# Optimization experiments

Hardware: AMD Instinct MI355X
Metric: run time of the kernel (lower is better)

## Reference

```python
import jax, jax.numpy as jnp
import numpy as np

N = 256  # image box size
B, P, L = 32, 300000, 64


def _gauss_kernel(sigma=1.0, size=5):
    ax = np.arange(size) - size // 2
    g = np.exp(-(ax ** 2) / (2.0 * sigma ** 2))
    k = np.outer(g, g)
    k = k / k.sum()
    return jnp.asarray(k, jnp.float32)


def _splat(cx, cy, w):
    # bilinear scatter-splat of P weighted points into [B, N, N] images
    x0 = jnp.floor(cx)
    y0 = jnp.floor(cy)
    fx = cx - x0
    fy = cy - y0
    xi0 = jnp.clip(x0.astype(jnp.int32), 0, N - 1)
    yi0 = jnp.clip(y0.astype(jnp.int32), 0, N - 1)
    xi1 = jnp.clip(xi0 + 1, 0, N - 1)
    yi1 = jnp.clip(yi0 + 1, 0, N - 1)
    b = jnp.broadcast_to(jnp.arange(cx.shape[0])[:, None], cx.shape)
    img = jnp.zeros((cx.shape[0], N, N), cx.dtype)
    img = img.at[b, yi0, xi0].add(w * (1 - fx) * (1 - fy))
    img = img.at[b, yi0, xi1].add(w * fx * (1 - fy))
    img = img.at[b, yi1, xi0].add(w * (1 - fx) * fy)
    img = img.at[b, yi1, xi1].add(w * fx * fy)
    return img


def setup_inputs() -> dict:
    key = jax.random.key(0)
    ks = jax.random.split(key, 9)
    z_x = jax.random.normal(ks[0], (B, L), jnp.float32)
    z_y = jax.random.normal(ks[1], (B, L), jnp.float32)
    z_z = jax.random.normal(ks[2], (B, L), jnp.float32)
    # Zernike basis scaled so deformations are a few pixels
    Z = 0.05 * jax.random.normal(ks[3], (P, L), jnp.float32)
    # masked volume point coordinates, centered, within +-N/4
    coords = (jax.random.uniform(ks[4], (P, 3), jnp.float32) - 0.5) * (0.5 * N)
    weights = jax.random.uniform(ks[5], (P,), jnp.float32)
    # proper per-image rotation matrices from random Euler angles (zyz)
    rng = np.random.RandomState(0)
    ang = rng.uniform(-np.pi, np.pi, (B, 3))
    ca, sa = np.cos(ang), np.sin(ang)
    Rm = np.zeros((B, 3, 3), np.float32)
    for i in range(B):
        a, b2, g = ang[i]
        Rz1 = np.array([[np.cos(a), -np.sin(a), 0], [np.sin(a), np.cos(a), 0], [0, 0, 1]])
        Ry = np.array([[np.cos(b2), 0, np.sin(b2)], [0, 1, 0], [-np.sin(b2), 0, np.cos(b2)]])
        Rz2 = np.array([[np.cos(g), -np.sin(g), 0], [np.sin(g), np.cos(g), 0], [0, 0, 1]])
        Rm[i] = (Rz1 @ Ry @ Rz2).astype(np.float32)
    R = jnp.asarray(Rm)
    shifts = 5.0 * jax.random.normal(ks[6], (B, 2), jnp.float32)
    # per-image radial CTF filter in Fourier space
    f = np.fft.fftfreq(N).astype(np.float32)
    r2 = f[:, None] ** 2 + f[None, :] ** 2  # [N, N]
    df = rng.uniform(500.0, 1500.0, (B, 1, 1)).astype(np.float32)
    ctf = jnp.asarray(np.sin(np.pi * df * r2[None]), jnp.float32)
    return {"z_x": z_x, "z_y": z_y, "z_z": z_z, "Z": Z, "coords": coords,
            "weights": weights, "R": R, "shifts": shifts, "ctf": ctf}


def reference(z_x, z_y, z_z, Z, coords, weights, R, shifts, ctf):
    # computeDeformationField: d = z @ Z^T -> [B, P]
    d_x = z_x @ Z.T
    d_y = z_y @ Z.T
    d_z = z_z @ Z.T
    # applyDeformationField: add reference coordinates per axis
    c_x = coords[:, 0][None, :] + d_x
    c_y = coords[:, 1][None, :] + d_y
    c_z = coords[:, 2][None, :] + d_z
    # applyAlignmentMatrix: per-image rotation, keep projected x/y rows
    c_r_x = R[:, 0, 0:1] * c_x + R[:, 0, 1:2] * c_y + R[:, 0, 2:3] * c_z
    c_r_y = R[:, 1, 0:1] * c_x + R[:, 1, 1:2] * c_y + R[:, 1, 2:3] * c_z
    # applyShifts: per-image shift + box-center offset
    half = jnp.float32(N / 2)
    px = c_r_x + shifts[:, 0:1] + half
    py = c_r_y + shifts[:, 1:2] + half
    # scatterImgByPass: bilinear scatter splat
    w = jnp.broadcast_to(weights[None, :], px.shape)
    img = _splat(px, py, w)  # [B, N, N]
    # gaussianFilterImage: 5x5 Gaussian blur
    k = _gauss_kernel()
    img_f = jax.lax.conv_general_dilated(
        img[:, None], k[None, None], (1, 1), 'SAME',
        dimension_numbers=('NCHW', 'OIHW', 'NCHW'))[:, 0]
    # ctfFilterImage: FFT multiply by real CTF, inverse FFT
    ft = jnp.fft.fft2(img_f)
    out = jnp.real(jnp.fft.ifft2(ft * ctf.astype(ft.dtype)))
    return out
```

## Files before the change

kernel.cpp:

```cpp
#include <hip/hip_runtime.h>
#include <hip/hip_bf16.h>

#define NIMG 32
#define NPTS 300000
#define NL   64
#define NBOX 256

#define BANDS  4
#define BROWS  64
#define CHUNKS 2
#define CHPTS  (NPTS / CHUNKS)

#define WQS  2047.0f
#define WQI  (1.0f / 2047.0f)

typedef float v2f __attribute__((ext_vector_type(2)));
typedef unsigned long long u64;

__device__ __forceinline__ int rev8(int x) { return (int)(__brev((unsigned)x) >> 24); }

__global__ __launch_bounds__(256) void zero_kernel(float4* p, int n4) {
    int i = blockIdx.x * 256 + threadIdx.x;
    if (i < n4) p[i] = make_float4(0.f, 0.f, 0.f, 0.f);
}

__global__ __launch_bounds__(256) void uvprep_kernel(
    const float* __restrict__ z_x, const float* __restrict__ z_y,
    const float* __restrict__ z_z, const float* __restrict__ R,
    const float* __restrict__ shifts,
    float* __restrict__ ubuf, float* __restrict__ vbuf, float4* __restrict__ hdrbuf)
{
    int t = threadIdx.x;
    for (int e = t; e < NIMG * NL; e += 256) {
        int b = e >> 6;
        const float* Rb = R + b * 9;
        float zx = z_x[e], zy = z_y[e], zz = z_z[e];
        ubuf[e] = Rb[0] * zx + Rb[1] * zy + Rb[2] * zz;
        vbuf[e] = Rb[3] * zx + Rb[4] * zy + Rb[5] * zz;
    }
    if (t < NIMG) {
        const float* Rb = R + t * 9;
        hdrbuf[2 * t]     = make_float4(Rb[0], Rb[1], Rb[2], shifts[2 * t]     + 128.f);
        hdrbuf[2 * t + 1] = make_float4(Rb[3], Rb[4], Rb[5], shifts[2 * t + 1] + 128.f);
    }
}

__global__ __launch_bounds__(256) void project_kernel(
    const float* __restrict__ Zb, const float* __restrict__ coords,
    const float* __restrict__ weights,
    const float* __restrict__ ubuf, const float* __restrict__ vbuf,
    const float4* __restrict__ hdrbuf,
    u64* __restrict__ recs)
{
    int tid = threadIdx.x;
    int p = blockIdx.x * 256 + tid;
    if (p >= NPTS) return;

    v2f zr[32];
    {
        const float4* Zr4 = (const float4*)(Zb + (size_t)p * NL);
        float4 tmp[16];
        #pragma unroll
        for (int i = 0; i < 16; ++i) tmp[i] = Zr4[i];
        const v2f* t2 = (const v2f*)tmp;
        #pragma unroll
        for (int i = 0; i < 32; ++i) zr[i] = t2[i];
    }

    float cx0 = coords[3 * p + 0];
    float cy0 = coords[3 * p + 1];
    float cz0 = coords[3 * p + 2];
    float w   = weights[p];

    for (int b = 0; b < NIMG; ++b) {
        float4 h0 = hdrbuf[2 * b], h1 = hdrbuf[2 * b + 1];
        const v2f* u2 = (const v2f*)(ubuf + b * NL);
        const v2f* v2 = (const v2f*)(vbuf + b * NL);
        v2f ax = {0.f, 0.f}, ay = {0.f, 0.f};
        #pragma unroll
        for (int i = 0; i < 32; ++i) {
            ax += u2[i] * zr[i];
            ay += v2[i] * zr[i];
        }
        float px = fmaf(h0.x, cx0, fmaf(h0.y, cy0, fmaf(h0.z, cz0, h0.w))) + ax.x + ax.y;
        float py = fmaf(h1.x, cx0, fmaf(h1.y, cy0, fmaf(h1.z, cz0, h1.w))) + ay.x + ay.y;

        float x0f = floorf(px), y0f = floorf(py);
        float fx = px - x0f, fy = py - y0f;
        int xi0 = min(max((int)x0f, 0), NBOX - 1);
        int yi0 = min(max((int)y0f, 0), NBOX - 1);
        float w00 = w * (1.f - fx) * (1.f - fy);
        float w10 = w * fx * (1.f - fy);
        float w01 = w * (1.f - fx) * fy;
        float w11 = w * fx * fy;
        if (xi0 == NBOX - 1) {
            w00 += w10; w10 = 0.f;
            w01 += w11; w11 = 0.f;
        }
        if (yi0 == NBOX - 1) {
            w00 += w01; w01 = 0.f;
            w10 += w11; w11 = 0.f;
        }
        u64 rec = (u64)(unsigned)(xi0 | (yi0 << 8))
                | ((u64)(unsigned)(w00 * WQS + 0.5f) << 16)
                | ((u64)(unsigned)(w10 * WQS + 0.5f) << 28)
                | ((u64)(unsigned)(w01 * WQS + 0.5f) << 40)
                | ((u64)(unsigned)(w11 * WQS + 0.5f) << 52);
        recs[(size_t)b * NPTS + p] = rec;
    }
}

__global__ __launch_bounds__(1024) void splat2_kernel(
    const u64* __restrict__ recs, float* __restrict__ img)
{
    __shared__ u64 VA[32 * 128];
    __shared__ u64 VB[32 * 129];
    __shared__ u64 VC[32 * 128];
    __shared__ u64 VD[32 * 129];
    int tid = threadIdx.x;
    int id = blockIdx.x;
    int band = id >> 6;
    int g    = id & 63;
    int b = g >> 1, c = g & 1;

    for (int i = tid; i < 32 * 128; i += 1024) { VA[i] = 0ULL; VC[i] = 0ULL; }
    for (int i = tid; i < 32 * 129; i += 1024) { VB[i] = 0ULL; VD[i] = 0ULL; }
    __syncthreads();

    const int y_lo = band * BROWS;
    const u64* rp = recs + (size_t)b * NPTS + (size_t)c * CHPTS;

    for (int i = 4 * tid; i < CHPTS; i += 4096) {
        ulonglong2 R01 = *(const ulonglong2*)(rp + i);
        ulonglong2 R23 = *(const ulonglong2*)(rp + i + 2);
        u64 Ra[4] = {R01.x, R01.y, R23.x, R23.y};
        #pragma unroll
        for (int k = 0; k < 4; ++k) {
            u64 rec = Ra[k];
            unsigned ps = (unsigned)rec & 0xFFFFu;
            int xi0 = ps & 255;
            int yi0 = ps >> 8;
            int r0 = yi0 - y_lo;
            if ((unsigned)r0 >= BROWS) continue;
            u64 val = ((rec >> 16) & 0xFFFULL)
                    | (((rec >> 28) & 0xFFFULL) << 16)
                    | (((rec >> 40) & 0xFFFULL) << 32)
                    | (((rec >> 52) & 0xFFFULL) << 48);
            int qr = r0 >> 1;
            int qc = (xi0 + (xi0 & 1)) >> 1;
            bool xodd = (xi0 & 1), yodd = (r0 & 1);
            u64* base = yodd ? (xodd ? VD : VC) : (xodd ? VB : VA);
            int stride = xodd ? 129 : 128;
            atomicAdd(&base[qr * stride + qc], val);
        }
    }
    __syncthreads();
    int nrows = min(BROWS + 1, NBOX - y_lo);
    float* ib = img + (size_t)b * NBOX * NBOX + (size_t)y_lo * NBOX;
    for (int i = tid; i < nrows * NBOX; i += 1024) {
        int r = i >> 8, x = i & 255;
        int fc0 = x & 1;
        int fc1 = fc0 ^ 1;
        int ja = x >> 1;
        int jb = (x + 1) >> 1;
        unsigned acc = 0;
        if (r < BROWS) {
            int fr = (r & 1) << 1;
            acc += (unsigned)((VA[(r >> 1) * 128 + ja] >> (16 * (fr | fc0))) & 0xFFFFu);
            acc += (unsigned)((VB[(r >> 1) * 129 + jb] >> (16 * (fr | fc1))) & 0xFFFFu);
        }
        if (r >= 1) {
            int fr = ((r & 1) ^ 1) << 1;
            acc += (unsigned)((VC[((r - 1) >> 1) * 128 + ja] >> (16 * (fr | fc0))) & 0xFFFFu);
            acc += (unsigned)((VD[((r - 1) >> 1) * 129 + jb] >> (16 * (fr | fc1))) & 0xFFFFu);
        }
        if (acc) unsafeAtomicAdd(ib + i, (float)acc * WQI);
    }
}

__global__ __launch_bounds__(256) void splat_kernel(
    const float* __restrict__ z_x, const float* __restrict__ z_y,
    const float* __restrict__ z_z, const float* __restrict__ Zb,
    const float* __restrict__ coords, const float* __restrict__ weights,
    const float* __restrict__ R, const float* __restrict__ shifts,
    float* __restrict__ img)
{
    __shared__ float s_z[3][NIMG][NL];
    __shared__ float s_R[NIMG][9];
    __shared__ float s_sh[NIMG][2];

    int tid = threadIdx.x;
    for (int i = tid; i < NIMG * NL; i += 256) {
        (&s_z[0][0][0])[i] = z_x[i];
        (&s_z[1][0][0])[i] = z_y[i];
        (&s_z[2][0][0])[i] = z_z[i];
    }
    for (int i = tid; i < NIMG * 9; i += 256) (&s_R[0][0])[i] = R[i];
    if (tid < NIMG * 2) (&s_sh[0][0])[tid] = shifts[tid];
    __syncthreads();

    int p = blockIdx.x * 256 + tid;
    if (p >= NPTS) return;

    float4 zr[16];
    const float4* Zr4 = (const float4*)(Zb + (size_t)p * NL);
    #pragma unroll
    for (int i = 0; i < 16; ++i) zr[i] = Zr4[i];

    float cx0 = coords[3 * p + 0];
    float cy0 = coords[3 * p + 1];
    float cz0 = coords[3 * p + 2];
    float w   = weights[p];

    for (int b = 0; b < NIMG; ++b) {
        const float4* zx4 = (const float4*)s_z[0][b];
        const float4* zy4 = (const float4*)s_z[1][b];
        const float4* zz4 = (const float4*)s_z[2][b];
        float dx = 0.f, dy = 0.f, dz = 0.f;
        #pragma unroll
        for (int i = 0; i < 16; ++i) {
            float4 a = zx4[i];
            dx += a.x * zr[i].x + a.y * zr[i].y + a.z * zr[i].z + a.w * zr[i].w;
            float4 bb = zy4[i];
            dy += bb.x * zr[i].x + bb.y * zr[i].y + bb.z * zr[i].z + bb.w * zr[i].w;
            float4 c = zz4[i];
            dz += c.x * zr[i].x + c.y * zr[i].y + c.z * zr[i].z + c.w * zr[i].w;
        }
        float cx = cx0 + dx, cy = cy0 + dy, cz = cz0 + dz;
        const float* Rb = s_R[b];
        float px = Rb[0] * cx + Rb[1] * cy + Rb[2] * cz + s_sh[b][0] + 128.0f;
        float py = Rb[3] * cx + Rb[4] * cy + Rb[5] * cz + s_sh[b][1] + 128.0f;

        float x0 = floorf(px), y0 = floorf(py);
        float fx = px - x0, fy = py - y0;
        int xi0 = min(max((int)x0, 0), NBOX - 1);
        int yi0 = min(max((int)y0, 0), NBOX - 1);
        int xi1 = min(xi0 + 1, NBOX - 1);
        int yi1 = min(yi0 + 1, NBOX - 1);

        float* ib = img + (size_t)b * NBOX * NBOX;
        unsafeAtomicAdd(ib + yi0 * NBOX + xi0, w * (1.f - fx) * (1.f - fy));
        unsafeAtomicAdd(ib + yi0 * NBOX + xi1, w * fx * (1.f - fy));
        unsafeAtomicAdd(ib + yi1 * NBOX + xi0, w * (1.f - fx) * fy);
        unsafeAtomicAdd(ib + yi1 * NBOX + xi1, w * fx * fy);
    }
}

__device__ __forceinline__ void fft_dif_t(float2* s, const float2* tw, int t) {
    #pragma unroll
    for (int st = 7; st >= 0; --st) {
        int half = 1 << st;
        int j  = t & (half - 1);
        int i1 = ((t >> st) << (st + 1)) + j;
        int i2 = i1 + half;
        float2 a = s[i1], b = s[i2];
        float2 w = tw[j << (7 - st)];
        float dxr = a.x - b.x, dxi = a.y - b.y;
        s[i1] = make_float2(a.x + b.x, a.y + b.y);
        s[i2] = make_float2(w.x * dxr - w.y * dxi, w.x * dxi + w.y * dxr);
        __syncthreads();
    }
}

__device__ __forceinline__ void fft_dit_t(float2* s, const float2* tw, int t) {
    #pragma unroll
    for (int st = 0; st < 8; ++st) {
        int half = 1 << st;
        int j  = t & (half - 1);
        int i1 = ((t >> st) << (st + 1)) + j;
        int i2 = i1 + half;
        float2 a = s[i1], b = s[i2];
        float2 w = tw[j << (7 - st)];
        float cs = w.x, sn = -w.y;
        float tr = cs * b.x - sn * b.y;
        float ti = cs * b.y + sn * b.x;
        s[i1] = make_float2(a.x + tr, a.y + ti);
        s[i2] = make_float2(a.x - tr, a.y - ti);
        __syncthreads();
    }
}

__device__ __forceinline__ void fft_dif_soa(float* re, float* im, const float2* tw, int t) {
    #pragma unroll
    for (int st = 7; st >= 0; --st) {
        int half = 1 << st;
        int j  = t & (half - 1);
        int i1 = ((t >> st) << (st + 1)) + j;
        int i2 = i1 + half;
        float ar = re[i1], ai = im[i1], br = re[i2], bi = im[i2];
        float2 w = tw[j << (7 - st)];
        float dr = ar - br, di = ai - bi;
        re[i1] = ar + br;  im[i1] = ai + bi;
        re[i2] = w.x * dr - w.y * di;
        im[i2] = w.x * di + w.y * dr;
        __syncthreads();
    }
}

__device__ __forceinline__ void fft_dit_soa(float* re, float* im, const float2* tw, int t) {
    #pragma unroll
    for (int st = 0; st < 8; ++st) {
        int half = 1 << st;
        int j  = t & (half - 1);
        int i1 = ((t >> st) << (st + 1)) + j;
        int i2 = i1 + half;
        float ar = re[i1], ai = im[i1], br = re[i2], bi = im[i2];
        float2 w = tw[j << (7 - st)];
        float cs = w.x, sn = -w.y;
        float tr = cs * br - sn * bi;
        float ti = cs * bi + sn * br;
        re[i1] = ar + tr;  im[i1] = ai + ti;
        re[i2] = ar - tr;  im[i2] = ai - ti;
        __syncthreads();
    }
}

__device__ __forceinline__ void init_tw(float2* tw, int tid) {
    if (tid < 128) {
        float sn, cs;
        sincosf(-6.283185307179586f * (float)tid * (1.0f / 256.0f), &sn, &cs);
        tw[tid] = make_float2(cs, sn);
    }
}

__global__ __launch_bounds__(256) void fft_rows_fwd_blur_kernel(const float* __restrict__ img,
                                                                float2* __restrict__ freq)
{
    __shared__ float2 s[2][NBOX];
    __shared__ float  sb[2][NBOX];
    __shared__ float2 tw[128];
    int tid = threadIdx.x;
    int tx = tid & 127, ty = tid >> 7;
    init_tw(tw, tid);
    int row = blockIdx.x * 2 + ty;
    int b = row >> 8, y = row & (NBOX - 1);
    const float* ib = img + ((size_t)b << 16);
    const float gw[5] = {0.0544886845f, 0.2442013420f, 0.4026199469f,
                         0.2442013420f, 0.0544886845f};
    float acc0 = 0.f, acc1 = 0.f;
    #pragma unroll
    for (int dy = -2; dy <= 2; ++dy) {
        int yy = y + dy;
        if ((unsigned)yy < (unsigned)NBOX) {
            const float* rp = ib + yy * NBOX;
            acc0 += gw[dy + 2] * rp[tx];
            acc1 += gw[dy + 2] * rp[tx + 128];
        }
    }
    sb[ty][tx] = acc0;  sb[ty][tx + 128] = acc1;
    __syncthreads();
    float r0 = 0.f, r1 = 0.f;
    #pragma unroll
    for (int dx = -2; dx <= 2; ++dx) {
        int x0 = tx + dx, x1 = tx + 128 + dx;
        if ((unsigned)x0 < (unsigned)NBOX) r0 += gw[dx + 2] * sb[ty][x0];
        if ((unsigned)x1 < (unsigned)NBOX) r1 += gw[dx + 2] * sb[ty][x1];
    }
    s[ty][tx]       = make_float2(r0, 0.f);
    s[ty][tx + 128] = make_float2(r1, 0.f);
    __syncthreads();
    fft_dif_t(s[ty], tw, tx);
    float2* op = freq + (size_t)row * NBOX;
    op[tx]       = s[ty][tx];
    op[tx + 128] = s[ty][tx + 128];
}

__global__ __launch_bounds__(1024) void fft_cols_ctf8_kernel(float2* __restrict__ freq,
                                                             const float* __restrict__ ctf)
{
    __shared__ float  s_re[8][257];
    __shared__ float  s_im[8][257];
    __shared__ float2 tw[128];
    int tid = threadIdx.x;
    init_tw(tw, tid);
    int col = tid & 7, j = tid >> 3;
    int blk = blockIdx.x;
    int b = blk >> 5;
    int x = ((blk & 31) << 3) + col;
    float2* base = freq + ((size_t)b << 16) + x;

    float2 v0 = base[(size_t)j * NBOX];
    float2 v1 = base[(size_t)(j + 128) * NBOX];
    s_re[col][j] = v0.x;        s_im[col][j] = v0.y;
    s_re[col][j + 128] = v1.x;  s_im[col][j + 128] = v1.y;
    __syncthreads();

    fft_dif_soa(s_re[col], s_im[col], tw, j);

    const float* cb = ctf + ((size_t)b << 16) + rev8(x);
    float c0 = cb[rev8(j) * NBOX];
    float c1 = cb[rev8(j + 128) * NBOX];
    s_re[col][j] *= c0;        s_im[col][j] *= c0;
    s_re[col][j + 128] *= c1;  s_im[col][j + 128] *= c1;
    __syncthreads();

    fft_dit_soa(s_re[col], s_im[col], tw, j);

    const float inv = 1.0f / 256.0f;
    base[(size_t)j * NBOX]         = make_float2(s_re[col][j] * inv, s_im[col][j] * inv);
    base[(size_t)(j + 128) * NBOX] = make_float2(s_re[col][j + 128] * inv, s_im[col][j + 128] * inv);
}

__global__ __launch_bounds__(256) void fft_rows_inv_kernel(const float2* __restrict__ freq,
                                                           float* __restrict__ out)
{
    __shared__ float2 s[2][NBOX];
    __shared__ float2 tw[128];
    int tid = threadIdx.x;
    int tx = tid & 127, ty = tid >> 7;
    init_tw(tw, tid);
    int row = blockIdx.x * 2 + ty;
    const float2* rp = freq + (size_t)row * NBOX;
    s[ty][tx]       = rp[tx];
    s[ty][tx + 128] = rp[tx + 128];
    __syncthreads();
    fft_dit_t(s[ty], tw, tx);
    const float inv = 1.0f / 256.0f;
    out[(size_t)row * NBOX + tx]       = s[ty][tx].x * inv;
    out[(size_t)row * NBOX + tx + 128] = s[ty][tx + 128].x * inv;
}

extern "C" void kernel_launch(void* const* d_in, const int* in_sizes, int n_in,
                              void* d_out, int out_size, void* d_ws, size_t ws_size,
                              hipStream_t stream)
{
    (void)in_sizes; (void)n_in; (void)out_size;
    const float* z_x     = (const float*)d_in[0];
    const float* z_y     = (const float*)d_in[1];
    const float* z_z     = (const float*)d_in[2];
    const float* Zb      = (const float*)d_in[3];
    const float* coords  = (const float*)d_in[4];
    const float* weights = (const float*)d_in[5];
    const float* R       = (const float*)d_in[6];
    const float* shifts  = (const float*)d_in[7];
    const float* ctf     = (const float*)d_in[8];
    float* out = (float*)d_out;

    const size_t NELEM = (size_t)NIMG * NBOX * NBOX;
    const size_t NPAIR = (size_t)NIMG * NPTS;
    char* base = (char*)d_ws;
    float* img  = (float*)base;
    u64*   recs = (u64*)(base + 8388608);
    float* ubuf = (float*)(base + 8388608 + 76800000);
    float* vbuf = ubuf + NIMG * NL;
    float4* hdrbuf = (float4*)(vbuf + NIMG * NL);
    float2* freq = (float2*)(base + 8388608);
    const size_t required = 8388608 + 76800000 + NIMG * NL * 8 + NIMG * 2 * 16;

    zero_kernel<<<(int)(NELEM / 4 + 255) / 256, 256, 0, stream>>>((float4*)img, (int)(NELEM / 4));

    if (ws_size >= required) {
        uvprep_kernel<<<1, 256, 0, stream>>>(z_x, z_y, z_z, R, shifts, ubuf, vbuf, hdrbuf);
        project_kernel<<<(NPTS + 255) / 256, 256, 0, stream>>>(Zb, coords, weights,
                                                               ubuf, vbuf, hdrbuf, recs);
        splat2_kernel<<<NIMG * BANDS * CHUNKS, 1024, 0, stream>>>(recs, img);
    } else {
        splat_kernel<<<(NPTS + 255) / 256, 256, 0, stream>>>(z_x, z_y, z_z, Zb, coords,
                                                             weights, R, shifts, img);
    }

    fft_rows_fwd_blur_kernel<<<NIMG * NBOX / 2, 256, 0, stream>>>(img, freq);
    fft_cols_ctf8_kernel<<<NIMG * 32, 1024, 0, stream>>>(freq, ctf);
    fft_rows_inv_kernel<<<NIMG * NBOX / 2, 256, 0, stream>>>(freq, out);
}
```

Measured before the change: 167.1 us.

## Compute point deformations with bf16 MFMA matrix cores instead of scalar FMAs

```diff
diff --git a/kernel.cpp b/kernel.cpp
--- a/kernel.cpp
+++ b/kernel.cpp
@@ -15,9 +15,17 @@
 #define WQI  (1.0f / 2047.0f)
 
 typedef float v2f __attribute__((ext_vector_type(2)));
+typedef float f32x4 __attribute__((ext_vector_type(4)));
+typedef short bf16x8 __attribute__((ext_vector_type(8)));
 typedef unsigned long long u64;
 
 __device__ __forceinline__ int rev8(int x) { return (int)(__brev((unsigned)x) >> 24); }
+
+__device__ __forceinline__ short f2bf(float f) {
+    unsigned u = __float_as_uint(f);
+    unsigned r = (u + 0x7FFFu + ((u >> 16) & 1u)) >> 16;
+    return (short)r;
+}
 
 __global__ __launch_bounds__(256) void zero_kernel(float4* p, int n4) {
     int i = blockIdx.x * 256 + threadIdx.x;
@@ -28,85 +36,130 @@
     const float* __restrict__ z_x, const float* __restrict__ z_y,
     const float* __restrict__ z_z, const float* __restrict__ R,
     const float* __restrict__ shifts,
-    float* __restrict__ ubuf, float* __restrict__ vbuf, float4* __restrict__ hdrbuf)
-{
+    float4* __restrict__ hdrbuf, short* __restrict__ Bt)
+{
+    __shared__ float s_u[NIMG * NL];
+    __shared__ float s_v[NIMG * NL];
     int t = threadIdx.x;
     for (int e = t; e < NIMG * NL; e += 256) {
         int b = e >> 6;
         const float* Rb = R + b * 9;
         float zx = z_x[e], zy = z_y[e], zz = z_z[e];
-        ubuf[e] = Rb[0] * zx + Rb[1] * zy + Rb[2] * zz;
-        vbuf[e] = Rb[3] * zx + Rb[4] * zy + Rb[5] * zz;
+        s_u[e] = Rb[0] * zx + Rb[1] * zy + Rb[2] * zz;
+        s_v[e] = Rb[3] * zx + Rb[4] * zy + Rb[5] * zz;
     }
     if (t < NIMG) {
         const float* Rb = R + t * 9;
         hdrbuf[2 * t]     = make_float4(Rb[0], Rb[1], Rb[2], shifts[2 * t]     + 128.f);
         hdrbuf[2 * t + 1] = make_float4(Rb[3], Rb[4], Rb[5], shifts[2 * t + 1] + 128.f);
     }
-}
-
-__global__ __launch_bounds__(256) void project_kernel(
+    __syncthreads();
+    for (int e = t; e < 64 * NL; e += 256) {
+        int c = e >> 6, k = e & 63;
+        int b = c >> 1;
+        float val = (c & 1) ? s_v[b * NL + k] : s_u[b * NL + k];
+        Bt[e] = f2bf(val);
+    }
+}
+
+__device__ __forceinline__ u64 make_rec(float px, float py, float w) {
+    float x0f = floorf(px), y0f = floorf(py);
+    float fx = px - x0f, fy = py - y0f;
+    int xi0 = min(max((int)x0f, 0), NBOX - 1);
+    int yi0 = min(max((int)y0f, 0), NBOX - 1);
+    float w00 = w * (1.f - fx) * (1.f - fy);
+    float w10 = w * fx * (1.f - fy);
+    float w01 = w * (1.f - fx) * fy;
+    float w11 = w * fx * fy;
+    if (xi0 == NBOX - 1) {
+        w00 += w10; w10 = 0.f;
+        w01 += w11; w11 = 0.f;
+    }
+    if (yi0 == NBOX - 1) {
+        w00 += w01; w01 = 0.f;
+        w10 += w11; w11 = 0.f;
+    }
+    return (u64)(unsigned)(xi0 | (yi0 << 8))
+         | ((u64)(unsigned)(w00 * WQS + 0.5f) << 16)
+         | ((u64)(unsigned)(w10 * WQS + 0.5f) << 28)
+         | ((u64)(unsigned)(w01 * WQS + 0.5f) << 40)
+         | ((u64)(unsigned)(w11 * WQS + 0.5f) << 52);
+}
+
+__global__ __launch_bounds__(256) void project_mfma_kernel(
     const float* __restrict__ Zb, const float* __restrict__ coords,
     const float* __restrict__ weights,
-    const float* __restrict__ ubuf, const float* __restrict__ vbuf,
-    const float4* __restrict__ hdrbuf,
+    const float4* __restrict__ hdrbuf, const short* __restrict__ Bt,
     u64* __restrict__ recs)
 {
     int tid = threadIdx.x;
-    int p = blockIdx.x * 256 + tid;
-    if (p >= NPTS) return;
-
-    v2f zr[32];
-    {
-        const float4* Zr4 = (const float4*)(Zb + (size_t)p * NL);
-        float4 tmp[16];
+    int lane = tid & 63;
+    int rg = (lane >> 4) & 3;
+    bool oddl = (lane & 1);
+
+    bf16x8 bf[4][2];
+    #pragma unroll
+    for (int t = 0; t < 4; ++t)
         #pragma unroll
-        for (int i = 0; i < 16; ++i) tmp[i] = Zr4[i];
-        const v2f* t2 = (const v2f*)tmp;
+        for (int q = 0; q < 2; ++q)
+            bf[t][q] = *(const bf16x8*)(Bt + (t * 16 + (lane & 15)) * NL + q * 32 + rg * 8);
+
+    int wid = blockIdx.x * 4 + (tid >> 6);
+    int nw  = gridDim.x * 4;
+    for (int mt = wid; mt < NPTS / 16; mt += nw) {
+        int pbase = mt * 16;
+        const float* zrow = Zb + (size_t)(pbase + (lane & 15)) * NL;
+        bf16x8 a[2];
         #pragma unroll
-        for (int i = 0; i < 32; ++i) zr[i] = t2[i];
-    }
-
-    float cx0 = coords[3 * p + 0];
-    float cy0 = coords[3 * p + 1];
-    float cz0 = coords[3 * p + 2];
-    float w   = weights[p];
-
-    for (int b = 0; b < NIMG; ++b) {
-        float4 h0 = hdrbuf[2 * b], h1 = hdrbuf[2 * b + 1];
-        const v2f* u2 = (const v2f*)(ubuf + b * NL);
-        const v2f* v2 = (const v2f*)(vbuf + b * NL);
-        v2f ax = {0.f, 0.f}, ay = {0.f, 0.f};
+        for (int q = 0; q < 2; ++q) {
+            float4 f0 = *(const float4*)(zrow + q * 32 + rg * 8);
+            float4 f1 = *(const float4*)(zrow + q * 32 + rg * 8 + 4);
+            bf16x8 av;
+            av[0] = f2bf(f0.x); av[1] = f2bf(f0.y); av[2] = f2bf(f0.z); av[3] = f2bf(f0.w);
+            av[4] = f2bf(f1.x); av[5] = f2bf(f1.y); av[6] = f2bf(f1.z); av[7] = f2bf(f1.w);
+            a[q] = av;
+        }
+        f32x4 accs[4];
         #pragma unroll
-        for (int i = 0; i < 32; ++i) {
-            ax += u2[i] * zr[i];
-            ay += v2[i] * zr[i];
-        }
-        float px = fmaf(h0.x, cx0, fmaf(h0.y, cy0, fmaf(h0.z, cz0, h0.w))) + ax.x + ax.y;
-        float py = fmaf(h1.x, cx0, fmaf(h1.y, cy0, fmaf(h1.z, cz0, h1.w))) + ay.x + ay.y;
-
-        float x0f = floorf(px), y0f = floorf(py);
-        float fx = px - x0f, fy = py - y0f;
-        int xi0 = min(max((int)x0f, 0), NBOX - 1);
-        int yi0 = min(max((int)y0f, 0), NBOX - 1);
-        float w00 = w * (1.f - fx) * (1.f - fy);
-        float w10 = w * fx * (1.f - fy);
-        float w01 = w * (1.f - fx) * fy;
-        float w11 = w * fx * fy;
-        if (xi0 == NBOX - 1) {
-            w00 += w10; w10 = 0.f;
-            w01 += w11; w11 = 0.f;
-        }
-        if (yi0 == NBOX - 1) {
-            w00 += w01; w01 = 0.f;
-            w10 += w11; w11 = 0.f;
-        }
-        u64 rec = (u64)(unsigned)(xi0 | (yi0 << 8))
-                | ((u64)(unsigned)(w00 * WQS + 0.5f) << 16)
-                | ((u64)(unsigned)(w10 * WQS + 0.5f) << 28)
-                | ((u64)(unsigned)(w01 * WQS + 0.5f) << 40)
-                | ((u64)(unsigned)(w11 * WQS + 0.5f) << 52);
-        recs[(size_t)b * NPTS + p] = rec;
+        for (int t = 0; t < 4; ++t) {
+            f32x4 acc = {0.f, 0.f, 0.f, 0.f};
+            acc = __builtin_amdgcn_mfma_f32_16x16x32_bf16(a[0], bf[t][0], acc, 0, 0, 0);
+            acc = __builtin_amdgcn_mfma_f32_16x16x32_bf16(a[1], bf[t][1], acc, 0, 0, 0);
+            accs[t] = acc;
+        }
+
+        int ra = rg * 4 + (oddl ? 2 : 0);
+        int pa = pbase + ra;
+        float cax = coords[3 * pa],     cay = coords[3 * pa + 1], caz = coords[3 * pa + 2];
+        float cbx = coords[3 * pa + 3], cby = coords[3 * pa + 4], cbz = coords[3 * pa + 5];
+        float wa = weights[pa], wb = weights[pa + 1];
+
+        #pragma unroll
+        for (int t = 0; t < 4; ++t) {
+            f32x4 acc = accs[t];
+            float o0 = __shfl_xor(acc[0], 1, 64);
+            float o1 = __shfl_xor(acc[1], 1, 64);
+            float o2 = __shfl_xor(acc[2], 1, 64);
+            float o3 = __shfl_xor(acc[3], 1, 64);
+            float m0 = oddl ? acc[2] : acc[0];
+            float m1 = oddl ? acc[3] : acc[1];
+            float t0 = oddl ? o2 : o0;
+            float t1 = oddl ? o3 : o1;
+            float dxa = oddl ? t0 : m0;
+            float dya = oddl ? m0 : t0;
+            float dxb = oddl ? t1 : m1;
+            float dyb = oddl ? m1 : t1;
+            int col = t * 16 + (lane & 15);
+            int img = col >> 1;
+            float4 h0 = hdrbuf[2 * img], h1 = hdrbuf[2 * img + 1];
+            float affxa = fmaf(h0.x, cax, fmaf(h0.y, cay, fmaf(h0.z, caz, h0.w)));
+            float affya = fmaf(h1.x, cax, fmaf(h1.y, cay, fmaf(h1.z, caz, h1.w)));
+            float affxb = fmaf(h0.x, cbx, fmaf(h0.y, cby, fmaf(h0.z, cbz, h0.w)));
+            float affyb = fmaf(h1.x, cbx, fmaf(h1.y, cby, fmaf(h1.z, cbz, h1.w)));
+            u64* pb = recs + (size_t)img * NPTS;
+            pb[pa]     = make_rec(affxa + dxa, affya + dya, wa);
+            pb[pa + 1] = make_rec(affxb + dxb, affyb + dyb, wb);
+        }
     }
 }
 
@@ -437,22 +490,20 @@
     float* out = (float*)d_out;
 
     const size_t NELEM = (size_t)NIMG * NBOX * NBOX;
-    const size_t NPAIR = (size_t)NIMG * NPTS;
     char* base = (char*)d_ws;
     float* img  = (float*)base;
     u64*   recs = (u64*)(base + 8388608);
-    float* ubuf = (float*)(base + 8388608 + 76800000);
-    float* vbuf = ubuf + NIMG * NL;
-    float4* hdrbuf = (float4*)(vbuf + NIMG * NL);
+    float4* hdrbuf = (float4*)(base + 8388608 + 76800000);
+    short*  Bt     = (short*)(base + 8388608 + 76800000 + 1024);
     float2* freq = (float2*)(base + 8388608);
-    const size_t required = 8388608 + 76800000 + NIMG * NL * 8 + NIMG * 2 * 16;
+    const size_t required = 8388608 + 76800000 + 1024 + 8192;
 
     zero_kernel<<<(int)(NELEM / 4 + 255) / 256, 256, 0, stream>>>((float4*)img, (int)(NELEM / 4));
 
     if (ws_size >= required) {
-        uvprep_kernel<<<1, 256, 0, stream>>>(z_x, z_y, z_z, R, shifts, ubuf, vbuf, hdrbuf);
-        project_kernel<<<(NPTS + 255) / 256, 256, 0, stream>>>(Zb, coords, weights,
-                                                               ubuf, vbuf, hdrbuf, recs);
+        uvprep_kernel<<<1, 256, 0, stream>>>(z_x, z_y, z_z, R, shifts, hdrbuf, Bt);
+        project_mfma_kernel<<<1024, 256, 0, stream>>>(Zb, coords, weights,
+                                                      hdrbuf, Bt, recs);
         splat2_kernel<<<NIMG * BANDS * CHUNKS, 1024, 0, stream>>>(recs, img);
     } else {
         splat_kernel<<<(NPTS + 255) / 256, 256, 0, stream>>>(z_x, z_y, z_z, Zb, coords,
```

New measurement: 150.7 us. 9.8% less time.
